# Kernel optimization log

Hardware: AMD Instinct MI355X
Metric: run time of the kernel (lower is better)

Reference implementation:

```python
import jax, jax.numpy as jnp
import numpy as np


def _dF(field, c):
    """Central differences of component c of field [B,X,Y,Z,C] -> [B,X-2,Y-2,Z-2,3]."""
    f = field[..., c]
    dx = (f[:, 2:, 1:-1, 1:-1] - f[:, :-2, 1:-1, 1:-1]) * 0.5
    dy = (f[:, 1:-1, 2:, 1:-1] - f[:, 1:-1, :-2, 1:-1]) * 0.5
    dz = (f[:, 1:-1, 1:-1, 2:] - f[:, 1:-1, 1:-1, :-2]) * 0.5
    return jnp.stack((dx, dy, dz), axis=4)


def setup_inputs() -> dict:
    key = jax.random.key(0)
    grid = jax.random.normal(key, (2, 160, 160, 160, 3), dtype=jnp.float32)
    return {"grid": grid}


def reference(grid):
    # First derivatives of each displacement component: [B,X-2,Y-2,Z-2,3]
    dx = _dF(grid, 0)
    dy = _dF(grid, 1)
    dz = _dF(grid, 2)
    # Second derivatives: [B,X-4,Y-4,Z-4,3]
    dxx = _dF(dx, 0)
    dyy = _dF(dy, 1)
    dzz = _dF(dz, 2)
    dxy = _dF(dx, 1)
    dyz = _dF(dy, 2)
    dxz = _dF(dx, 2)
    penalty = jnp.sum(dxx ** 2 + dyy ** 2 + dzz ** 2
                      + 2.0 * (dxy ** 2 + dyz ** 2 + dxz ** 2))
    return penalty / dxx.size
```

## Files before the change

kernel.cpp:

```cpp
#include <hip/hip_runtime.h>

#define OY 480
#define OX 76800
#define SB 12288000
#define SUBW 60
#define ROWW 180
#define SLICE 3060
#define NBUF 6
#define NCHUNK 714
#define NBLK 504
#define INV_SIZE (1.0f/22778496.0f)

#define LD8(dst, p)  { *(float4*)(dst) = *(const float4*)(p); \
                       *(float4*)((dst)+4) = *(const float4*)((p)+4); }
#define LD4Z(dst, p) { *(float2*)(dst) = *(const float2*)((p)+2); \
                       *(float2*)((dst)+2) = *(const float2*)((p)+4); }

__global__ __launch_bounds__(256, 2)
void be_partials(const float* __restrict__ g, float* __restrict__ partial) {
    __shared__ float lds[NBUF * SLICE];
    __shared__ float wsum[4];

    const int tid  = threadIdx.x;
    const int bid  = blockIdx.x;
    const int iseg = bid % 7;
    int r = bid / 7;
    const int kt = r % 3; r /= 3;
    const int jt = r % 12;
    const int bb = r / 12;
    const int j0  = jt * 13;
    const int kf0 = kt * 156;
    const int i0  = (iseg < 2) ? 23 * iseg : 46 + 22 * (iseg - 2);
    const int len = (iseg < 2) ? 23 : 22;

    const float* __restrict__ G = g + (size_t)bb * SB;

    int goff[3], loff[3][4];
    bool have2;
    #pragma unroll
    for (int c = 0; c < 3; ++c) {
        const int cid = tid + 256 * c;
        const int row = cid / 42, q = cid - row * 42;
        goff[c] = (j0 + row) * OY + kf0 + 4 * q;
        #pragma unroll
        for (int m = 0; m < 4; ++m) {
            const int gf = 4 * q + m;
            const int zl = gf / 3;
            const int cc = gf - 3 * zl;
            loff[c][m] = row * ROWW + cc * SUBW + zl;
        }
    }
    have2 = tid < (NCHUNK - 512);

    const bool act = tid < 169;
    const int jj = act ? tid / 13 : 0;
    const int ss = act ? (tid - jj * 13) : 0;
    const int rb = (jj + 2) * ROWW;
    const int wb = 4 * ss;

    for (int w = 0; w < 5; ++w) {
        const float* base = G + (size_t)(i0 + w) * OX;
        float* L = lds + ((i0 + w) % NBUF) * SLICE;
        #pragma unroll
        for (int c = 0; c < 3; ++c) {
            if (c < 2 || have2) {
                float4 v = *(const float4*)(base + goff[c]);
                L[loff[c][0]] = v.x; L[loff[c][1]] = v.y;
                L[loff[c][2]] = v.z; L[loff[c][3]] = v.w;
            }
        }
    }
    __syncthreads();

    float w1 = 0.f, w2 = 0.f, w3 = 0.f, w4 = 0.f;
    for (int t = 0; t < len; ++t) {
        const int cg = i0 + 2 + t;
        const bool doLoad = t < len - 1;
        float4 v0 = make_float4(0,0,0,0), v1 = v0, v2 = v0;
        if (doLoad) {
            const float* base = G + (size_t)(cg + 3) * OX;
            v0 = *(const float4*)(base + goff[0]);
            v1 = *(const float4*)(base + goff[1]);
            if (have2) v2 = *(const float4*)(base + goff[2]);
        }

        if (act) {
            const float* S0 = lds + ((cg - 2) % NBUF) * SLICE;
            const float* S1 = lds + ((cg - 1) % NBUF) * SLICE;
            const float* S2 = lds + ((cg    ) % NBUF) * SLICE;
            const float* S3 = lds + ((cg + 1) % NBUF) * SLICE;
            const float* S4 = lds + ((cg + 2) % NBUF) * SLICE;

            float A[8], Bv[8], Cv[8];
            const float* cr = S2 + rb + wb;
            LD8(A,  cr); LD8(Bv, cr + SUBW); LD8(Cv, cr + 2*SUBW);
            #pragma unroll
            for (int q = 0; q < 4; ++q) {
                float hzz0 = A[4+q]  - 2.f*A[2+q]  + A[q];
                float hzz1 = Bv[4+q] - 2.f*Bv[2+q] + Bv[q];
                float hzz2 = Cv[4+q] - 2.f*Cv[2+q] + Cv[q];
                w2 = fmaf(hzz0, hzz0, w2);
                w2 = fmaf(hzz1, hzz1, w2);
                w1 = fmaf(hzz2, hzz2, w1);
            }
            {
                const float* up = S2 + rb + ROWW + wb;
                const float* dn = S2 + rb - ROWW + wb;
                float P[8], M[8];
                LD8(P, up); LD8(M, dn);
                #pragma unroll
                for (int q = 0; q < 4; ++q) {
                    float h = (P[3+q] - P[1+q]) - (M[3+q] - M[1+q]);
                    w4 = fmaf(h, h, w4);
                }
                LD8(P, up + SUBW); LD8(M, dn + SUBW);
                #pragma unroll
                for (int q = 0; q < 4; ++q) {
                    float h = (P[3+q] - P[1+q]) - (M[3+q] - M[1+q]);
                    w3 = fmaf(h, h, w3);
                }
                LD8(P, up + 2*SUBW); LD8(M, dn + 2*SUBW);
                #pragma unroll
                for (int q = 0; q < 4; ++q) {
                    float h = (P[3+q] - P[1+q]) - (M[3+q] - M[1+q]);
                    w1 = fmaf(h, h, w1);
                }
            }
            {
                const float* up = S2 + rb + 2*ROWW + wb;
                const float* dn = S2 + rb - 2*ROWW + wb;
                float P0[4], M0[4], P1[4], M1[4];
                LD4Z(P0, up); LD4Z(M0, dn);
                LD4Z(P1, up + SUBW); LD4Z(M1, dn + SUBW);
                #pragma unroll
                for (int q = 0; q < 4; ++q) {
                    float h0 = P0[q] - 2.f*A[2+q]  + M0[q];
                    float h1 = P1[q] - 2.f*Bv[2+q] + M1[q];
                    w2 = fmaf(h0, h0, w2);
                    w1 = fmaf(h1, h1, w1);
                }
            }
            {
                const float* pp = S3 + rb + wb;
                const float* mm = S1 + rb + wb;
                float P[8], M[8];
                LD8(P, pp); LD8(M, mm);
                #pragma unroll
                for (int q = 0; q < 4; ++q) {
                    float h = (P[3+q] - P[1+q]) - (M[3+q] - M[1+q]);
                    w3 = fmaf(h, h, w3);
                }
                LD8(P, pp + SUBW); LD8(M, mm + SUBW);
                #pragma unroll
                for (int q = 0; q < 4; ++q) {
                    float h = (P[3+q] - P[1+q]) - (M[3+q] - M[1+q]);
                    w2 = fmaf(h, h, w2);
                }
                LD8(P, pp + 2*SUBW); LD8(M, mm + 2*SUBW);
                #pragma unroll
                for (int q = 0; q < 4; ++q) {
                    float h = (P[3+q] - P[1+q]) - (M[3+q] - M[1+q]);
                    w1 = fmaf(h, h, w1);
                }
            }
            {
                const float* pu = S3 + rb + ROWW + wb;
                const float* pd = S3 + rb - ROWW + wb;
                const float* mu = S1 + rb + ROWW + wb;
                const float* md = S1 + rb - ROWW + wb;
                float a[4], b[4], c[4], d[4];
                LD4Z(a, pu); LD4Z(b, pd); LD4Z(c, mu); LD4Z(d, md);
                #pragma unroll
                for (int q = 0; q < 4; ++q) {
                    float h = (a[q] - b[q]) - (c[q] - d[q]);
                    w3 = fmaf(h, h, w3);
                }
                LD4Z(a, pu + SUBW); LD4Z(b, pd + SUBW);
                LD4Z(c, mu + SUBW); LD4Z(d, md + SUBW);
                #pragma unroll
                for (int q = 0; q < 4; ++q) {
                    float h = (a[q] - b[q]) - (c[q] - d[q]);
                    w1 = fmaf(h, h, w1);
                }
            }
            {
                float p[4], m[4];
                LD4Z(p, S4 + rb + wb); LD4Z(m, S0 + rb + wb);
                #pragma unroll
                for (int q = 0; q < 4; ++q) {
                    float h = p[q] - 2.f*A[2+q] + m[q];
                    w1 = fmaf(h, h, w1);
                }
            }
        }

        if (doLoad) {
            float* L = lds + ((cg + 3) % NBUF) * SLICE;
            L[loff[0][0]] = v0.x; L[loff[0][1]] = v0.y;
            L[loff[0][2]] = v0.z; L[loff[0][3]] = v0.w;
            L[loff[1][0]] = v1.x; L[loff[1][1]] = v1.y;
            L[loff[1][2]] = v1.z; L[loff[1][3]] = v1.w;
            if (have2) {
                L[loff[2][0]] = v2.x; L[loff[2][1]] = v2.y;
                L[loff[2][2]] = v2.z; L[loff[2][3]] = v2.w;
            }
        }
        __syncthreads();
    }

    float s = fmaf(2.f, w2, w1);
    s = fmaf(3.f, w3, s);
    s = fmaf(4.f, w4, s);
    s *= 0.0625f;

    #pragma unroll
    for (int off = 32; off > 0; off >>= 1) s += __shfl_down(s, off, 64);
    if ((tid & 63) == 0) wsum[tid >> 6] = s;
    __syncthreads();
    if (tid == 0)
        partial[bid] = (wsum[0] + wsum[1]) + (wsum[2] + wsum[3]);
}

__global__ __launch_bounds__(256)
void be_final(const float* __restrict__ partial, float* __restrict__ out) {
    float s = 0.0f;
    for (int i = threadIdx.x; i < NBLK; i += 256) s += partial[i];
    #pragma unroll
    for (int off = 32; off > 0; off >>= 1) s += __shfl_down(s, off, 64);
    __shared__ float ws[4];
    if ((threadIdx.x & 63) == 0) ws[threadIdx.x >> 6] = s;
    __syncthreads();
    if (threadIdx.x == 0)
        out[0] = ((ws[0] + ws[1]) + (ws[2] + ws[3])) * INV_SIZE;
}

extern "C" void kernel_launch(void* const* d_in, const int* in_sizes, int n_in,
                              void* d_out, int out_size, void* d_ws, size_t ws_size,
                              hipStream_t stream) {
    const float* grid = (const float*)d_in[0];
    float* out = (float*)d_out;
    float* partials = (float*)d_ws;

    be_partials<<<dim3(NBLK), dim3(256), 0, stream>>>(grid, partials);
    be_final<<<1, 256, 0, stream>>>(partials, out);
}
```

Before: 172.3 us.

## Cache x-stencil rows in registers and restage LDS with vectorized component-planar layout

```diff
diff --git a/kernel.cpp b/kernel.cpp
--- a/kernel.cpp
+++ b/kernel.cpp
@@ -3,11 +3,10 @@
 #define OY 480
 #define OX 76800
 #define SB 12288000
-#define SUBW 60
-#define ROWW 180
-#define SLICE 3060
+#define ZP 56
+#define CP 952
+#define SLICE 2856
 #define NBUF 6
-#define NCHUNK 714
 #define NBLK 504
 #define INV_SIZE (1.0f/22778496.0f)
 
@@ -24,188 +23,174 @@
     const int tid  = threadIdx.x;
     const int bid  = blockIdx.x;
     const int iseg = bid % 7;
-    int r = bid / 7;
-    const int kt = r % 3; r /= 3;
-    const int jt = r % 12;
-    const int bb = r / 12;
+    int r_ = bid / 7;
+    const int kt = r_ % 3;  r_ /= 3;
+    const int jt = r_ % 12;
+    const int bb = r_ / 12;
     const int j0  = jt * 13;
     const int kf0 = kt * 156;
-    const int i0  = (iseg < 2) ? 23 * iseg : 46 + 22 * (iseg - 2);
-    const int len = (iseg < 2) ? 23 : 22;
+    const int i0  = iseg * 24;
+    const int len = (iseg == 6) ? 12 : 24;
 
     const float* __restrict__ G = g + (size_t)bb * SB;
 
-    int goff[3], loff[3][4];
-    bool have2;
-    #pragma unroll
-    for (int c = 0; c < 3; ++c) {
-        const int cid = tid + 256 * c;
-        const int row = cid / 42, q = cid - row * 42;
-        goff[c] = (j0 + row) * OY + kf0 + 4 * q;
-        #pragma unroll
-        for (int m = 0; m < 4; ++m) {
-            const int gf = 4 * q + m;
-            const int zl = gf / 3;
-            const int cc = gf - 3 * zl;
-            loff[c][m] = row * ROWW + cc * SUBW + zl;
-        }
-    }
-    have2 = tid < (NCHUNK - 512);
+    const bool stg = tid < 238;
+    int srow = 0, st14 = 0;
+    if (stg) { srow = tid / 14; st14 = tid - srow * 14; }
+    const int goff = (j0 + srow) * OY + kf0 + 12 * st14;
+    const int lw   = srow * ZP + 4 * st14;
 
     const bool act = tid < 169;
-    const int jj = act ? tid / 13 : 0;
-    const int ss = act ? (tid - jj * 13) : 0;
-    const int rb = (jj + 2) * ROWW;
-    const int wb = 4 * ss;
+    int jj = act ? tid / 13 : 0;
+    int ss = act ? tid - jj * 13 : 0;
+    const int rbase = (jj + 2) * ZP + 4 * ss;
+
+    float a0[6][8], a1[3][8], a2[3][8];
 
     for (int w = 0; w < 5; ++w) {
-        const float* base = G + (size_t)(i0 + w) * OX;
-        float* L = lds + ((i0 + w) % NBUF) * SLICE;
-        #pragma unroll
-        for (int c = 0; c < 3; ++c) {
-            if (c < 2 || have2) {
-                float4 v = *(const float4*)(base + goff[c]);
-                L[loff[c][0]] = v.x; L[loff[c][1]] = v.y;
-                L[loff[c][2]] = v.z; L[loff[c][3]] = v.w;
-            }
+        if (stg) {
+            const float* base = G + (size_t)(i0 + w) * OX + goff;
+            float4 q0 = *(const float4*)(base);
+            float4 q1 = *(const float4*)(base + 4);
+            float4 q2 = *(const float4*)(base + 8);
+            float* L = lds + w * SLICE + lw;
+            *(float4*)(L)        = make_float4(q0.x, q0.w, q1.z, q2.y);
+            *(float4*)(L + CP)   = make_float4(q0.y, q1.x, q1.w, q2.z);
+            *(float4*)(L + 2*CP) = make_float4(q0.z, q1.y, q2.x, q2.w);
         }
     }
     __syncthreads();
+    if (act) {
+        #pragma unroll
+        for (int s = 0; s < 4; ++s) LD8(a0[s], lds + s * SLICE + rbase);
+        #pragma unroll
+        for (int s = 1; s <= 2; ++s) {
+            LD8(a1[s], lds + s * SLICE + CP + rbase);
+            LD8(a2[s], lds + s * SLICE + 2*CP + rbase);
+        }
+    }
 
     float w1 = 0.f, w2 = 0.f, w3 = 0.f, w4 = 0.f;
-    for (int t = 0; t < len; ++t) {
-        const int cg = i0 + 2 + t;
-        const bool doLoad = t < len - 1;
-        float4 v0 = make_float4(0,0,0,0), v1 = v0, v2 = v0;
-        if (doLoad) {
-            const float* base = G + (size_t)(cg + 3) * OX;
-            v0 = *(const float4*)(base + goff[0]);
-            v1 = *(const float4*)(base + goff[1]);
-            if (have2) v2 = *(const float4*)(base + goff[2]);
-        }
-
-        if (act) {
-            const float* S0 = lds + ((cg - 2) % NBUF) * SLICE;
-            const float* S1 = lds + ((cg - 1) % NBUF) * SLICE;
-            const float* S2 = lds + ((cg    ) % NBUF) * SLICE;
-            const float* S3 = lds + ((cg + 1) % NBUF) * SLICE;
-            const float* S4 = lds + ((cg + 2) % NBUF) * SLICE;
-
-            float A[8], Bv[8], Cv[8];
-            const float* cr = S2 + rb + wb;
-            LD8(A,  cr); LD8(Bv, cr + SUBW); LD8(Cv, cr + 2*SUBW);
-            #pragma unroll
-            for (int q = 0; q < 4; ++q) {
-                float hzz0 = A[4+q]  - 2.f*A[2+q]  + A[q];
-                float hzz1 = Bv[4+q] - 2.f*Bv[2+q] + Bv[q];
-                float hzz2 = Cv[4+q] - 2.f*Cv[2+q] + Cv[q];
-                w2 = fmaf(hzz0, hzz0, w2);
-                w2 = fmaf(hzz1, hzz1, w2);
-                w1 = fmaf(hzz2, hzz2, w1);
+    for (int tb = 0; tb < len; tb += 6) {
+        #pragma unroll
+        for (int U = 0; U < 6; ++U) {
+            const int t  = tb + U;
+            const int cg = i0 + 2 + t;
+            const bool doLoad = (t < len - 1);
+            float4 q0, q1, q2;
+            if (doLoad && stg) {
+                const float* base = G + (size_t)(cg + 3) * OX + goff;
+                q0 = *(const float4*)(base);
+                q1 = *(const float4*)(base + 4);
+                q2 = *(const float4*)(base + 8);
             }
-            {
-                const float* up = S2 + rb + ROWW + wb;
-                const float* dn = S2 + rb - ROWW + wb;
-                float P[8], M[8];
-                LD8(P, up); LD8(M, dn);
+
+            if (act) {
+                const int sc   = (2 + U) % 6;
+                const int sp1  = (3 + U) % 6;
+                const int sp2  = (4 + U) % 6;
+                const int sm1  = (1 + U) % 6;
+                const int sm2  = (U) % 6;
+                const int ic   = (2 + U) % 3;
+                const int ip1  = (U) % 3;
+                const int im1  = (1 + U) % 3;
+
+                LD8(a0[sp2], lds + sp2 * SLICE + rbase);
+                LD8(a1[ip1], lds + sp1 * SLICE + CP + rbase);
+                LD8(a2[ip1], lds + sp1 * SLICE + 2*CP + rbase);
+
+                const float* S1 = lds + sm1 * SLICE;
+                const float* S2 = lds + sc  * SLICE;
+                const float* S3 = lds + sp1 * SLICE;
+
+                const float* A0c = a0[sc];  const float* A0p = a0[sp1];
+                const float* A0m = a0[sm1]; const float* A0P = a0[sp2];
+                const float* A0M = a0[sm2];
+                const float* A1c = a1[ic];  const float* A1p = a1[ip1];
+                const float* A1m = a1[im1];
+                const float* A2c = a2[ic];  const float* A2p = a2[ip1];
+                const float* A2m = a2[im1];
+
                 #pragma unroll
                 for (int q = 0; q < 4; ++q) {
-                    float h = (P[3+q] - P[1+q]) - (M[3+q] - M[1+q]);
-                    w4 = fmaf(h, h, w4);
-                }
-                LD8(P, up + SUBW); LD8(M, dn + SUBW);
-                #pragma unroll
-                for (int q = 0; q < 4; ++q) {
-                    float h = (P[3+q] - P[1+q]) - (M[3+q] - M[1+q]);
-                    w3 = fmaf(h, h, w3);
-                }
-                LD8(P, up + 2*SUBW); LD8(M, dn + 2*SUBW);
-                #pragma unroll
-                for (int q = 0; q < 4; ++q) {
-                    float h = (P[3+q] - P[1+q]) - (M[3+q] - M[1+q]);
-                    w1 = fmaf(h, h, w1);
+                    float hzz0 = A0c[q+4] - 2.f*A0c[q+2] + A0c[q];
+                    float hzz1 = A1c[q+4] - 2.f*A1c[q+2] + A1c[q];
+                    float hzz2 = A2c[q+4] - 2.f*A2c[q+2] + A2c[q];
+                    w2 = fmaf(hzz0, hzz0, w2);
+                    w2 = fmaf(hzz1, hzz1, w2);
+                    w1 = fmaf(hzz2, hzz2, w1);
+                    float hxx0 = A0P[q+2] - 2.f*A0c[q+2] + A0M[q+2];
+                    w1 = fmaf(hxx0, hxx0, w1);
+                    float hxz0 = (A0p[q+3] - A0p[q+1]) - (A0m[q+3] - A0m[q+1]);
+                    float hxz1 = (A1p[q+3] - A1p[q+1]) - (A1m[q+3] - A1m[q+1]);
+                    float hxz2 = (A2p[q+3] - A2p[q+1]) - (A2m[q+3] - A2m[q+1]);
+                    w3 = fmaf(hxz0, hxz0, w3);
+                    w2 = fmaf(hxz1, hxz1, w2);
+                    w1 = fmaf(hxz2, hxz2, w1);
+                }
+                {
+                    float P[8], M[8];
+                    LD8(P, S2 + rbase + ZP); LD8(M, S2 + rbase - ZP);
+                    #pragma unroll
+                    for (int q = 0; q < 4; ++q) {
+                        float h = (P[q+3] - P[q+1]) - (M[q+3] - M[q+1]);
+                        w4 = fmaf(h, h, w4);
+                    }
+                    LD8(P, S2 + CP + rbase + ZP); LD8(M, S2 + CP + rbase - ZP);
+                    #pragma unroll
+                    for (int q = 0; q < 4; ++q) {
+                        float h = (P[q+3] - P[q+1]) - (M[q+3] - M[q+1]);
+                        w3 = fmaf(h, h, w3);
+                    }
+                    LD8(P, S2 + 2*CP + rbase + ZP); LD8(M, S2 + 2*CP + rbase - ZP);
+                    #pragma unroll
+                    for (int q = 0; q < 4; ++q) {
+                        float h = (P[q+3] - P[q+1]) - (M[q+3] - M[q+1]);
+                        w1 = fmaf(h, h, w1);
+                    }
+                }
+                {
+                    float Pz[4], Mz[4];
+                    LD4Z(Pz, S2 + rbase + 2*ZP); LD4Z(Mz, S2 + rbase - 2*ZP);
+                    #pragma unroll
+                    for (int q = 0; q < 4; ++q) {
+                        float h = Pz[q] - 2.f*A0c[q+2] + Mz[q];
+                        w2 = fmaf(h, h, w2);
+                    }
+                    LD4Z(Pz, S2 + CP + rbase + 2*ZP); LD4Z(Mz, S2 + CP + rbase - 2*ZP);
+                    #pragma unroll
+                    for (int q = 0; q < 4; ++q) {
+                        float h = Pz[q] - 2.f*A1c[q+2] + Mz[q];
+                        w1 = fmaf(h, h, w1);
+                    }
+                }
+                {
+                    float av[4], bv[4], cv[4], dv[4];
+                    LD4Z(av, S3 + rbase + ZP); LD4Z(bv, S3 + rbase - ZP);
+                    LD4Z(cv, S1 + rbase + ZP); LD4Z(dv, S1 + rbase - ZP);
+                    #pragma unroll
+                    for (int q = 0; q < 4; ++q) {
+                        float h = (av[q] - bv[q]) - (cv[q] - dv[q]);
+                        w3 = fmaf(h, h, w3);
+                    }
+                    LD4Z(av, S3 + CP + rbase + ZP); LD4Z(bv, S3 + CP + rbase - ZP);
+                    LD4Z(cv, S1 + CP + rbase + ZP); LD4Z(dv, S1 + CP + rbase - ZP);
+                    #pragma unroll
+                    for (int q = 0; q < 4; ++q) {
+                        float h = (av[q] - bv[q]) - (cv[q] - dv[q]);
+                        w1 = fmaf(h, h, w1);
+                    }
                 }
             }
-            {
-                const float* up = S2 + rb + 2*ROWW + wb;
-                const float* dn = S2 + rb - 2*ROWW + wb;
-                float P0[4], M0[4], P1[4], M1[4];
-                LD4Z(P0, up); LD4Z(M0, dn);
-                LD4Z(P1, up + SUBW); LD4Z(M1, dn + SUBW);
-                #pragma unroll
-                for (int q = 0; q < 4; ++q) {
-                    float h0 = P0[q] - 2.f*A[2+q]  + M0[q];
-                    float h1 = P1[q] - 2.f*Bv[2+q] + M1[q];
-                    w2 = fmaf(h0, h0, w2);
-                    w1 = fmaf(h1, h1, w1);
-                }
+
+            if (doLoad && stg) {
+                float* L = lds + ((5 + U) % 6) * SLICE + lw;
+                *(float4*)(L)        = make_float4(q0.x, q0.w, q1.z, q2.y);
+                *(float4*)(L + CP)   = make_float4(q0.y, q1.x, q1.w, q2.z);
+                *(float4*)(L + 2*CP) = make_float4(q0.z, q1.y, q2.x, q2.w);
             }
-            {
-                const float* pp = S3 + rb + wb;
-                const float* mm = S1 + rb + wb;
-                float P[8], M[8];
-                LD8(P, pp); LD8(M, mm);
-                #pragma unroll
-                for (int q = 0; q < 4; ++q) {
-                    float h = (P[3+q] - P[1+q]) - (M[3+q] - M[1+q]);
-                    w3 = fmaf(h, h, w3);
-                }
-                LD8(P, pp + SUBW); LD8(M, mm + SUBW);
-                #pragma unroll
-                for (int q = 0; q < 4; ++q) {
-                    float h = (P[3+q] - P[1+q]) - (M[3+q] - M[1+q]);
-                    w2 = fmaf(h, h, w2);
-                }
-                LD8(P, pp + 2*SUBW); LD8(M, mm + 2*SUBW);
-                #pragma unroll
-                for (int q = 0; q < 4; ++q) {
-                    float h = (P[3+q] - P[1+q]) - (M[3+q] - M[1+q]);
-                    w1 = fmaf(h, h, w1);
-                }
-            }
-            {
-                const float* pu = S3 + rb + ROWW + wb;
-                const float* pd = S3 + rb - ROWW + wb;
-                const float* mu = S1 + rb + ROWW + wb;
-                const float* md = S1 + rb - ROWW + wb;
-                float a[4], b[4], c[4], d[4];
-                LD4Z(a, pu); LD4Z(b, pd); LD4Z(c, mu); LD4Z(d, md);
-                #pragma unroll
-                for (int q = 0; q < 4; ++q) {
-                    float h = (a[q] - b[q]) - (c[q] - d[q]);
-                    w3 = fmaf(h, h, w3);
-                }
-                LD4Z(a, pu + SUBW); LD4Z(b, pd + SUBW);
-                LD4Z(c, mu + SUBW); LD4Z(d, md + SUBW);
-                #pragma unroll
-                for (int q = 0; q < 4; ++q) {
-                    float h = (a[q] - b[q]) - (c[q] - d[q]);
-                    w1 = fmaf(h, h, w1);
-                }
-            }
-            {
-                float p[4], m[4];
-                LD4Z(p, S4 + rb + wb); LD4Z(m, S0 + rb + wb);
-                #pragma unroll
-                for (int q = 0; q < 4; ++q) {
-                    float h = p[q] - 2.f*A[2+q] + m[q];
-                    w1 = fmaf(h, h, w1);
-                }
-            }
+            __syncthreads();
         }
-
-        if (doLoad) {
-            float* L = lds + ((cg + 3) % NBUF) * SLICE;
-            L[loff[0][0]] = v0.x; L[loff[0][1]] = v0.y;
-            L[loff[0][2]] = v0.z; L[loff[0][3]] = v0.w;
-            L[loff[1][0]] = v1.x; L[loff[1][1]] = v1.y;
-            L[loff[1][2]] = v1.z; L[loff[1][3]] = v1.w;
-            if (have2) {
-                L[loff[2][0]] = v2.x; L[loff[2][1]] = v2.y;
-                L[loff[2][2]] = v2.z; L[loff[2][3]] = v2.w;
-            }
-        }
-        __syncthreads();
     }
 
     float s = fmaf(2.f, w2, w1);
```

After: 176.6 us. +2.5%, slower.
